# Kernel tuning notes

Hardware: AMD Instinct MI355X
Metric: run time of the kernel (lower is better)

The kernel has to match this reference:

```python
import jax, jax.numpy as jnp
from jax import lax
import numpy as np

M = 128      # number of hidden states
D = 8        # observation dim
T = 131072   # sequence length
LOG2PI = float(np.log(2.0 * np.pi))


def setup_inputs() -> dict:
    key = jax.random.key(0)
    k1, k2, k3, k4, k5 = jax.random.split(key, 5)
    y = jax.random.normal(k1, (T, D), dtype=jnp.float32)
    transition_logits = jax.random.normal(k2, (M, M - 1), dtype=jnp.float32)
    init_logits = jax.random.normal(k3, (M,), dtype=jnp.float32)
    means = jax.random.normal(k4, (M, D), dtype=jnp.float32)
    log_sigmas = 0.1 * jax.random.normal(k5, (M, D), dtype=jnp.float32)
    return {"y": y, "transition_logits": transition_logits,
            "init_logits": init_logits, "means": means, "log_sigmas": log_sigmas}


def _build_gamma(transition_logits):
    # (m, m-1) free logits; diagonal logit pinned to 0, then row softmax.
    m = transition_logits.shape[0]
    rows, cols = np.where(~np.eye(m, dtype=bool))  # static indices
    full = jnp.zeros((m, m), transition_logits.dtype).at[rows, cols].set(
        transition_logits.reshape(-1))
    return jax.nn.softmax(full, axis=-1)


def _log_emission(y, means, log_sigmas):
    # logg[t, j] = sum_d log N(y[t,d]; mu[j,d], sigma[j,d])  -> (T, m)
    z = (y[:, None, :] - means[None]) * jnp.exp(-log_sigmas)[None]  # (T, m, D)
    return -0.5 * jnp.sum(z * z + 2.0 * log_sigmas[None] + LOG2PI, axis=-1)


def reference(y, transition_logits, init_logits, means, log_sigmas):
    Gamma = _build_gamma(transition_logits)          # (m, m)
    u0 = jax.nn.softmax(init_logits)                 # initial state dist
    g = jnp.exp(_log_emission(y, means, log_sigmas))  # (T, m) emission densities

    def step(u_prev, gt):
        u_t = u_prev @ Gamma            # predict
        f_t = jnp.sum(u_t * gt)         # normalizer (per-step likelihood)
        u_tt = u_t * gt / f_t           # filtered posterior
        return u_tt, (u_tt, f_t, u_t)

    _, (Ut, ft, Utt) = lax.scan(step, u0, g)
    # matches original: Ut = stacked filtered dists, ft = normalizers, Utt = predicted dists
    return Ut, ft, Utt
```

## Files before the change

### kernel.cpp

```cpp
#include <hip/hip_runtime.h>
#include <math.h>

#define MST   128
#define DOBS  8
#define TLEN  131072
#define LOG2PI_F 1.8378770664093453f

#define CLEN  8
#define NW    (TLEN / CLEN / 16)
#define WARM  16
#define NSTEP (WARM + CLEN)
#define GPAD  128
#define EROWS 16

typedef __attribute__((ext_vector_type(8))) short v8s;
typedef __attribute__((ext_vector_type(4))) float v4f;
typedef __attribute__((ext_vector_type(4))) unsigned int v4u;

__device__ __forceinline__ unsigned short f2bf_rne(float x) {
  unsigned int b = __builtin_bit_cast(unsigned int, x);
  unsigned int r = b + 0x7FFFu + ((b >> 16) & 1u);
  return (unsigned short)(r >> 16);
}
__device__ __forceinline__ unsigned cvtpk(float a, float b) {
  unsigned r;
  asm("v_cvt_pk_bf16_f32 %0, %1, %2" : "=v"(r) : "v"(a), "v"(b));
  return r;
}
__device__ __forceinline__ float bflo(unsigned u) {
  return __builtin_bit_cast(float, u << 16);
}
__device__ __forceinline__ float bfhi(unsigned u) {
  return __builtin_bit_cast(float, u & 0xFFFF0000u);
}

__global__ void build_params(const float* __restrict__ tl,
                             const float* __restrict__ il,
                             const float* __restrict__ ls,
                             float* __restrict__ Gf,
                             float* __restrict__ u0,
                             float* __restrict__ isb,
                             float* __restrict__ cstb) {
  __shared__ float red[MST];
  const int j = threadIdx.x;
  const int b = blockIdx.x;
  float lg;
  if (b < MST) lg = (j == b) ? 0.0f : tl[b * (MST - 1) + (j > b ? j - 1 : j)];
  else         lg = il[j];
  float e = __expf(lg);
  red[j] = e;
  __syncthreads();
  for (int s = MST / 2; s > 0; s >>= 1) {
    if (j < s) red[j] += red[j + s];
    __syncthreads();
  }
  float val = e / red[0];
  if (b < MST) {
    Gf[b * MST + j] = val;
  } else {
    u0[j] = val;
    float c = -((float)DOBS * 0.5f) * LOG2PI_F;
#pragma unroll
    for (int d = 0; d < DOBS; ++d) {
      float l = ls[j * DOBS + d];
      isb[j * DOBS + d] = __expf(-l);
      c -= l;
    }
    cstb[j] = c;
  }
}

__global__ void build_afrag(const float* __restrict__ Gf,
                            unsigned short* __restrict__ GA) {
  const int idx = blockIdx.x * 64 + threadIdx.x;
  const int l  = idx & 63;
  const int mk = idx >> 6;
  const int kt = mk & 3, m = mk >> 2;
  const int i  = l & 15, hh = l >> 4;
  const int rg = 16 * m + i;
  const int lam = ((rg >> 5) << 5) | (((rg >> 2) & 3) << 3) | (((rg >> 4) & 1) << 2) | (rg & 3);
  unsigned short o[8];
#pragma unroll
  for (int j = 0; j < 8; ++j) {
    const int src = 32 * kt + 8 * hh + j;
    o[j] = f2bf_rne(Gf[src * MST + lam]);
  }
  *(v4u*)(GA + (size_t)idx * 8) = *(const v4u*)o;
}

__global__ void emis_kernel(const float* __restrict__ y,
                            const float* __restrict__ mu,
                            const float* __restrict__ isb,
                            const float* __restrict__ cstb,
                            unsigned short* __restrict__ g0) {
  const int lb = ((blockIdx.x & 7) << 10) | (blockIdx.x >> 3);
  const int j  = threadIdx.x;
  const int tb = lb * EROWS;
  __shared__ float ysh[EROWS * DOBS];
  ysh[j] = y[(unsigned)tb * DOBS + j];
  __syncthreads();
  float m[DOBS], is[DOBS];
  float cst = cstb[j];
#pragma unroll
  for (int d = 0; d < DOBS; ++d) { m[d] = mu[j * DOBS + d]; is[d] = isb[j * DOBS + d]; }
#pragma unroll
  for (int r = 0; r < EROWS; ++r) {
    float q = 0.0f;
#pragma unroll
    for (int d = 0; d < DOBS; ++d) {
      float z = (ysh[r * DOBS + d] - m[d]) * is[d];
      q = fmaf(z, z, q);
    }
    g0[(unsigned)(tb + r) * MST + j] = f2bf_rne(__expf(fmaf(-0.5f, q, cst)));
  }
}

__device__ __forceinline__ void packBh(const v4f* w, v8s* Bh) {
#pragma unroll
  for (int kt = 0; kt < 4; ++kt) {
    const v4f wa = w[2 * kt], wb = w[2 * kt + 1];
    Bh[kt] = __builtin_bit_cast(v8s, (v4u){cvtpk(wa[0], wa[1]), cvtpk(wa[2], wa[3]),
                                           cvtpk(wb[0], wb[1]), cvtpk(wb[2], wb[3])});
  }
}

__device__ __forceinline__ void step(
    int n, int wid, int c, int h,
    const v8s* A, v8s* Bh, v4u (&cur)[4],
    float& inv, unsigned& gvo, unsigned& uvo,
    const char* gbase, const float* u0,
    char* outUt, char* outF, char* outUtt) {
  const bool live = n >= WARM;

  v4f D[8] = {};
#pragma unroll
  for (int kt = 0; kt < 4; ++kt)
#pragma unroll
    for (int m = 0; m < 8; ++m)
      D[m] = __builtin_amdgcn_mfma_f32_16x16x32_bf16(A[m * 4 + kt], Bh[kt], D[m], 0, 0, 0);

  v4f gci[8];
#pragma unroll
  for (int mm = 0; mm < 4; ++mm) {
    const v4u raw = cur[mm];
    gci[2 * mm + 0] = (v4f){bflo(raw.x), bfhi(raw.x), bflo(raw.y), bfhi(raw.y)} * inv;
    gci[2 * mm + 1] = (v4f){bflo(raw.z), bfhi(raw.z), bflo(raw.w), bfhi(raw.w)} * inv;
  }

#pragma unroll
  for (int mm = 0; mm < 4; ++mm)
    cur[mm] = *(const v4u*)(gbase + (gvo + (unsigned)mm * 64u));
  gvo += 256u;

  if (live) {
#pragma unroll
    for (int m = 0; m < 8; ++m) {
      v4f p = D[m] * inv;
      *(v4f*)(outUtt + (uvo + (m >> 1) * 128 + (m & 1) * 16)) = p;
    }
  }
  v4f w[8];
#pragma unroll
  for (int m = 0; m < 8; ++m) w[m] = D[m] * gci[m];

  if (wid == 0 && n < WARM && ((n & 7) == 7)) {
    const int ctar = (WARM - 1 - n) >> 3;
#pragma unroll
    for (int m = 0; m < 8; ++m) {
      v4f uv = *(const v4f*)(u0 + (m >> 1) * 32 + h * 8 + (m & 1) * 4);
      if (c == ctar) w[m] = uv;
    }
  }

  v4f a0 = w[0] + w[1], a1 = w[2] + w[3], a2 = w[4] + w[5], a3 = w[6] + w[7];
  v4f a6 = (a0 + a1) + (a2 + a3);
  float s = (a6[0] + a6[1]) + (a6[2] + a6[3]);
  s += __shfl_xor(s, 16);
  s += __shfl_xor(s, 32);
  const float invn = __builtin_amdgcn_rcpf(s);

  packBh(w, Bh);

  if (live) {
#pragma unroll
    for (int m = 0; m < 8; ++m) {
      v4f ut = w[m] * invn;
      *(v4f*)(outUt + (uvo + (m >> 1) * 128 + (m & 1) * 16)) = ut;
    }
    if (h == 0) *(float*)(outF + (uvo >> 7)) = s;
  }
  uvo += 512u;
  inv = invn;
}

__global__ __launch_bounds__(64, 1)
void hmm_scan(const char* __restrict__ gbase,
              const unsigned short* __restrict__ GA,
              const float* __restrict__ u0,
              char* __restrict__ outUt,
              char* __restrict__ outF,
              char* __restrict__ outUtt) {
  const int l = threadIdx.x;
  const int h = l >> 4, c = l & 15;
  const int wid = ((blockIdx.x & 7) << 7) | (blockIdx.x >> 3);
  const int t00 = (wid * 16 + c) * CLEN;
  const int t0  = t00 - WARM;

  v8s A[32];
#pragma unroll
  for (int f = 0; f < 32; ++f)
    A[f] = *(const v8s*)(GA + (size_t)(f * 64 + l) * 8);

  v4f w[8];
#pragma unroll
  for (int m = 0; m < 8; ++m)
    w[m] = (v4f){1.0f / MST, 1.0f / MST, 1.0f / MST, 1.0f / MST};
  if (wid == 0 && c == (WARM / CLEN)) {
#pragma unroll
    for (int m = 0; m < 8; ++m)
      w[m] = *(const v4f*)(u0 + (m >> 1) * 32 + h * 8 + (m & 1) * 4);
  }
  float inv = 1.0f;

  v8s Bh[4];
  packBh(w, Bh);

  unsigned gvo = (unsigned)((t0 + GPAD) * 256 + h * 16);
  v4u gA[4], gB[4], gC[4];
#pragma unroll
  for (int mm = 0; mm < 4; ++mm) {
    gA[mm] = *(const v4u*)(gbase + (gvo + (unsigned)mm * 64u));
    gB[mm] = *(const v4u*)(gbase + (gvo + 256u + (unsigned)mm * 64u));
    gC[mm] = *(const v4u*)(gbase + (gvo + 512u + (unsigned)mm * 64u));
  }
  gvo += 768u;
  unsigned uvo = (unsigned)(t0 * 512 + h * 32);

#define SARG wid, c, h, A, Bh
#define TAIL inv, gvo, uvo, gbase, u0, outUt, outF, outUtt
#pragma clang loop unroll(disable)
  for (int n = 0; n < 24; n += 3) {
    step(n + 0, SARG, gA, TAIL);
    step(n + 1, SARG, gB, TAIL);
    step(n + 2, SARG, gC, TAIL);
  }
#undef SARG
#undef TAIL
}

extern "C" void kernel_launch(void* const* d_in, const int* in_sizes, int n_in,
                              void* d_out, int out_size, void* d_ws, size_t ws_size,
                              hipStream_t stream) {
  const float* y  = (const float*)d_in[0];
  const float* tl = (const float*)d_in[1];
  const float* il = (const float*)d_in[2];
  const float* mu = (const float*)d_in[3];
  const float* ls = (const float*)d_in[4];

  unsigned short* gf16 = (unsigned short*)d_ws;
  unsigned short* g0   = gf16 + (size_t)GPAD * MST;
  float* u0 = (float*)(gf16 + (size_t)(TLEN + 2 * GPAD) * MST);
  float* Gf = u0 + MST;
  unsigned short* GA = (unsigned short*)(Gf + MST * MST);
  float* isb  = (float*)(GA + 32 * 64 * 8);
  float* cstb = isb + MST * DOBS;

  char* outUt  = (char*)d_out;
  char* outF   = outUt + (size_t)TLEN * MST * 4;
  char* outUtt = outF + (size_t)TLEN * 4;

  build_params<<<MST + 1, MST, 0, stream>>>(tl, il, ls, Gf, u0, isb, cstb);
  build_afrag<<<32, 64, 0, stream>>>(Gf, GA);
  emis_kernel<<<TLEN / EROWS, MST, 0, stream>>>(y, mu, isb, cstb, g0);
  hmm_scan<<<NW, 64, 0, stream>>>((const char*)gf16, GA, u0, outUt, outF, outUtt);
}
```

Baseline: 68.57 us.

## Stage Ut/Utt outputs through swizzled LDS for coalesced 512B-row stores

Instead of each lane writing scattered 16-byte fragments of its chunk's output rows directly to global memory, each step writes the predicted and filtered vectors into XOR-swizzled shared-memory buffers. Each lane then reads them back and issues fully contiguous stores covering whole 512-byte rows for pairs of chunks. The goal is better global write coalescing for the dominant output traffic, at the cost of extra LDS writes and reads per step. No barrier separates the LDS writes from the reads; this relies on the block being a single wavefront executing in lockstep.

Result: no change. 67.99 us (-0.8%).

```diff
diff --git a/kernel.cpp b/kernel.cpp
--- a/kernel.cpp
+++ b/kernel.cpp
@@ -125,11 +125,13 @@
 }
 
 __device__ __forceinline__ void step(
-    int n, int wid, int c, int h,
+    int n, int wid, int c, int h, int j32, int cg,
     const v8s* A, v8s* Bh, v4u (&cur)[4],
-    float& inv, unsigned& gvo, unsigned& uvo,
+    float& inv, unsigned& gvo,
     const char* gbase, const float* u0,
-    char* outUt, char* outF, char* outUtt) {
+    char* LUt, char* LUtt,
+    char* outUt, char* outF, char* outUtt,
+    unsigned sbase, unsigned foff) {
   const bool live = n >= WARM;
 
   v4f D[8] = {};
@@ -156,7 +158,8 @@
 #pragma unroll
     for (int m = 0; m < 8; ++m) {
       v4f p = D[m] * inv;
-      *(v4f*)(outUtt + (uvo + (m >> 1) * 128 + (m & 1) * 16)) = p;
+      const int s = ((m >> 1) << 3) | (h << 1) | (m & 1);
+      *(v4f*)(LUtt + (c << 9) + ((s ^ c) << 4)) = p;
     }
   }
   v4f w[8];
@@ -185,11 +188,23 @@
 #pragma unroll
     for (int m = 0; m < 8; ++m) {
       v4f ut = w[m] * invn;
-      *(v4f*)(outUt + (uvo + (m >> 1) * 128 + (m & 1) * 16)) = ut;
-    }
-    if (h == 0) *(float*)(outF + (uvo >> 7)) = s;
-  }
-  uvo += 512u;
+      const int sl = ((m >> 1) << 3) | (h << 1) | (m & 1);
+      *(v4f*)(LUt + (c << 9) + ((sl ^ c) << 4)) = ut;
+    }
+    const unsigned d = (unsigned)(n - WARM);
+    if (h == 0) *(float*)(outF + foff + d * 4u) = s;
+    unsigned off = sbase + d * 512u;
+#pragma unroll
+    for (int i = 0; i < 8; ++i) {
+      const int ci = 2 * i + cg;
+      const unsigned lo = (unsigned)(ci << 9) + (unsigned)((j32 ^ ci) << 4);
+      v4f pa = *(const v4f*)(LUtt + lo);
+      v4f ua = *(const v4f*)(LUt + lo);
+      *(v4f*)(outUtt + off) = pa;
+      *(v4f*)(outUt + off) = ua;
+      off += 8192u;
+    }
+  }
   inv = invn;
 }
 
@@ -200,11 +215,18 @@
               char* __restrict__ outUt,
               char* __restrict__ outF,
               char* __restrict__ outUtt) {
+  __shared__ __align__(16) char LUt[16 * 512];
+  __shared__ __align__(16) char LUtt[16 * 512];
+
   const int l = threadIdx.x;
   const int h = l >> 4, c = l & 15;
+  const int j32 = l & 31, cg = l >> 5;
   const int wid = ((blockIdx.x & 7) << 7) | (blockIdx.x >> 3);
   const int t00 = (wid * 16 + c) * CLEN;
   const int t0  = t00 - WARM;
+
+  const unsigned sbase = (unsigned)(wid * 16 + cg) * 4096u + (unsigned)j32 * 16u;
+  const unsigned foff  = (unsigned)((wid * 16 + c) * CLEN) * 4u;
 
   v8s A[32];
 #pragma unroll
@@ -234,10 +256,9 @@
     gC[mm] = *(const v4u*)(gbase + (gvo + 512u + (unsigned)mm * 64u));
   }
   gvo += 768u;
-  unsigned uvo = (unsigned)(t0 * 512 + h * 32);
-
-#define SARG wid, c, h, A, Bh
-#define TAIL inv, gvo, uvo, gbase, u0, outUt, outF, outUtt
+
+#define SARG wid, c, h, j32, cg, A, Bh
+#define TAIL inv, gvo, gbase, u0, LUt, LUtt, outUt, outF, outUtt, sbase, foff
 #pragma clang loop unroll(disable)
   for (int n = 0; n < 24; n += 3) {
     step(n + 0, SARG, gA, TAIL);
```
